# Kernel tuning notes

Measured on AMD Instinct MI355X. Metric: run time of the kernel, lower is better.

Reference implementation:

```python
import jax, jax.numpy as jnp
import numpy as np

# NF4 codebook used by bitsandbytes (16 levels, normalized to [-1, 1])
NF4_CODE = jnp.array([
    -1.0, -0.6961928009986877, -0.5250730514526367, -0.39491748809814453,
    -0.28444138169288635, -0.18477343022823334, -0.09105003625154495, 0.0,
    0.07958029955625534, 0.16093020141124725, 0.24611230194568634,
    0.33791524171829224, 0.44070982933044434, 0.5626170039176941,
    0.7229568362236023, 1.0], dtype=jnp.float32)
BLOCKSIZE = 64  # bitsandbytes default 4-bit blocksize


def nf4_quant_dequant(w):
    """Simulate bnb NF4 quantize -> dequantize (per-block absmax scaling)."""
    shape = w.shape
    flat = w.reshape(-1, BLOCKSIZE)                     # [n_blocks, 64]
    absmax = jnp.max(jnp.abs(flat), axis=1, keepdims=True)
    normalized = flat / jnp.where(absmax == 0, 1.0, absmax)
    # nearest-codebook-value quantization via midpoint boundaries
    bounds = (NF4_CODE[:-1] + NF4_CODE[1:]) * 0.5       # [15]
    idx = jnp.searchsorted(bounds, normalized)          # [n_blocks, 64] in [0,15]
    return (NF4_CODE[idx] * absmax).reshape(shape)


def setup_inputs() -> dict:
    key = jax.random.key(0)
    k1, k2, k3, kx = jax.random.split(key, 4)
    D, H = 4096, 11008
    scale = 0.02  # typical transformer init scale
    w1 = jax.random.normal(k1, (H, D), jnp.float32) * scale
    w2 = jax.random.normal(k2, (H, D), jnp.float32) * scale
    w3 = jax.random.normal(k3, (D, H), jnp.float32) * scale
    x = jax.random.normal(kx, (2, 2048, D), jnp.float32)
    return {"x": x, "w1": w1, "w2": w2, "w3": w3}


def reference(x, w1, w2, w3):
    dq1 = nf4_quant_dequant(w1)   # [H, D]
    dq2 = nf4_quant_dequant(w2)   # [H, D]
    dq3 = nf4_quant_dequant(w3)   # [D, H]
    gate = jnp.einsum('bsd,hd->bsh', x, dq1)
    up = jnp.einsum('bsd,hd->bsh', x, dq2)
    h = jax.nn.silu(gate) * up
    return jnp.einsum('bsh,dh->bsd', h, dq3)
```

## Files before the change

kernel.cpp:

```cpp
#include <hip/hip_runtime.h>
#include <math.h>

typedef __attribute__((ext_vector_type(4))) float f32x4;
typedef __attribute__((ext_vector_type(8))) short bf16x8;

#define DI __device__ __forceinline__

DI unsigned short f32_to_bf16(float f) {
  unsigned int u = __float_as_uint(f);
  u += 0x7FFFu + ((u >> 16) & 1u);
  return (unsigned short)(u >> 16);
}

static constexpr float kCode[16] = {
    -1.0f, -0.6961928009986877f, -0.5250730514526367f, -0.39491748809814453f,
    -0.28444138169288635f, -0.18477343022823334f, -0.09105003625154495f, 0.0f,
    0.07958029955625534f, 0.16093020141124725f, 0.24611230194568634f,
    0.33791524171829224f, 0.44070982933044434f, 0.5626170039176941f,
    0.7229568362236023f, 1.0f};

DI void dequant_body(const float* __restrict__ in, unsigned short* __restrict__ out, int i) {
  f32x4 v = reinterpret_cast<const f32x4*>(in)[i];
  float am = fmaxf(fmaxf(fabsf(v.x), fabsf(v.y)), fmaxf(fabsf(v.z), fabsf(v.w)));
  am = fmaxf(am, __shfl_xor(am, 1));
  am = fmaxf(am, __shfl_xor(am, 2));
  am = fmaxf(am, __shfl_xor(am, 4));
  am = fmaxf(am, __shfl_xor(am, 8));
  const float scale = (am == 0.0f) ? 1.0f : am;
  float sb[15];
#pragma unroll
  for (int b = 0; b < 15; ++b)
    sb[b] = (0.5f * (kCode[b] + kCode[b + 1])) * scale;
  unsigned short o[4];
#pragma unroll
  for (int j = 0; j < 4; ++j) {
    const float vj = ((const float*)&v)[j];
    int idx = 0;
#pragma unroll
    for (int b = 0; b < 15; ++b)
      idx += (vj > sb[b]) ? 1 : 0;
    o[j] = f32_to_bf16(kCode[idx] * am);
  }
  reinterpret_cast<ushort4*>(out)[i] = make_ushort4(o[0], o[1], o[2], o[3]);
}

__global__ void __launch_bounds__(256) k_dequant_nf4(
    const float* __restrict__ in, unsigned short* __restrict__ out, int n4) {
  int i = blockIdx.x * 256 + threadIdx.x;
  if (i >= n4) return;
  dequant_body(in, out, i);
}

__global__ void __launch_bounds__(256) k_aux_all(
    const float* __restrict__ x, unsigned short* __restrict__ xb, int n4x,
    const float* __restrict__ w1, unsigned short* __restrict__ w1b,
    const float* __restrict__ w2, unsigned short* __restrict__ w2b, int n4w) {
  int i = blockIdx.x * 256 + threadIdx.x;
  if (i < n4x) {
    f32x4 v = reinterpret_cast<const f32x4*>(x)[i];
    reinterpret_cast<ushort4*>(xb)[i] =
        make_ushort4(f32_to_bf16(v.x), f32_to_bf16(v.y), f32_to_bf16(v.z), f32_to_bf16(v.w));
  } else if (i < n4x + n4w) {
    dequant_body(w1, w1b, i - n4x);
  } else {
    dequant_body(w2, w2b, i - n4x - n4w);
  }
}

DI void gload16(const void* g, void* l) {
  __builtin_amdgcn_global_load_lds(
      (const __attribute__((address_space(1))) void*)g,
      (__attribute__((address_space(3))) void*)l, 16, 0, 0);
}

DI void barrier_nodrain() {
  asm volatile("" ::: "memory");
  __builtin_amdgcn_s_barrier();
  asm volatile("" ::: "memory");
}

#define WAITV(N) asm volatile("s_waitcnt vmcnt(" #N ")" ::: "memory")

DI float fast_silu(float g) {
  const float e = __builtin_amdgcn_exp2f(g * -1.442695041f);
  return g * __builtin_amdgcn_rcpf(1.0f + e);
}

__global__ void __launch_bounds__(1024, 4) k_gemm_dual_swiglu(
    const unsigned short* __restrict__ X,
    const unsigned short* __restrict__ W1,
    const unsigned short* __restrict__ W2,
    unsigned short* __restrict__ H) {
  constexpr int K = 4096, N = 11008, NK = K / 32;
  __shared__ char ldsb[131072];

  const int tid = threadIdx.x;
  const int w = tid >> 6, l = tid & 63;

  const int bid = blockIdx.x;
  const int xcd = bid & 7, ii = bid >> 3;
  const int nt = ii >> 1;
  const int mt = xcd * 2 + (ii & 1);
  const int m0 = mt * 256, n0 = nt * 128;

  const int p = w & 7;
  const bool isGate = (w < 8);
  const int wr = p >> 1, wc = p & 1;

  const int lrow = l >> 2;
  const int kc8 = (((l & 3) ^ ((l >> 3) & 3)) << 3);
  const unsigned short* gsrc0;
  const unsigned short* gsrc1;
  int ldst0;
  if (w < 8) {
    gsrc0 = X + (size_t)(m0 + 32 * w + lrow) * K + kc8;
    gsrc1 = X + (size_t)(m0 + 32 * w + 16 + lrow) * K + kc8;
    ldst0 = 2 * w * 1024;
  } else if (w < 12) {
    gsrc0 = W1 + (size_t)(n0 + 32 * (w - 8) + lrow) * K + kc8;
    gsrc1 = W1 + (size_t)(n0 + 32 * (w - 8) + 16 + lrow) * K + kc8;
    ldst0 = 16384 + (w - 8) * 2048;
  } else {
    gsrc0 = W2 + (size_t)(n0 + 32 * (w - 12) + lrow) * K + kc8;
    gsrc1 = W2 + (size_t)(n0 + 32 * (w - 12) + 16 + lrow) * K + kc8;
    ldst0 = 24576 + (w - 12) * 2048;
  }

  const int roff = (((l >> 4) ^ ((l >> 1) & 3)) << 4);
  const char* rdA = ldsb + (wr * 64 + (l & 15)) * 64 + roff;
  const char* rdB = ldsb + 16384 + (isGate ? 0 : 8192) +
                    (wc * 64 + (l & 15)) * 64 + roff;

  f32x4 acc[4][4] = {};

#define TILE_BODY(bo) {                                                        \
  bf16x8 a[4], b[4];                                                           \
  _Pragma("unroll") for (int m = 0; m < 4; ++m)                                \
    a[m] = *(const bf16x8*)(rdA + (bo) + m * 1024);                            \
  _Pragma("unroll") for (int n = 0; n < 4; ++n)                                \
    b[n] = *(const bf16x8*)(rdB + (bo) + n * 1024);                            \
  _Pragma("unroll") for (int m = 0; m < 4; ++m)                                \
    _Pragma("unroll") for (int n = 0; n < 4; ++n)                              \
      acc[m][n] = __builtin_amdgcn_mfma_f32_16x16x32_bf16(a[m], b[n], acc[m][n], 0, 0, 0); }

  gload16(gsrc0, ldsb + ldst0);               gload16(gsrc1, ldsb + ldst0 + 1024);
  gload16(gsrc0 + 32, ldsb + 32768 + ldst0);  gload16(gsrc1 + 32, ldsb + 32768 + ldst0 + 1024);
  gload16(gsrc0 + 64, ldsb + 65536 + ldst0);  gload16(gsrc1 + 64, ldsb + 65536 + ldst0 + 1024);
  const unsigned short* pg0 = gsrc0 + 96;
  const unsigned short* pg1 = gsrc1 + 96;
  WAITV(4);
  barrier_nodrain();

  int t = 0;
  for (; t + 3 < NK; ++t) {
    const int bo = (t & 3) << 15;
    const int bs = ((t + 3) & 3) << 15;
    gload16(pg0, ldsb + bs + ldst0);
    gload16(pg1, ldsb + bs + ldst0 + 1024);
    pg0 += 32; pg1 += 32;
    TILE_BODY(bo);
    WAITV(4); barrier_nodrain();
  }
  TILE_BODY((t & 3) << 15); WAITV(2); barrier_nodrain(); ++t;
  TILE_BODY((t & 3) << 15); WAITV(0); barrier_nodrain(); ++t;
  TILE_BODY((t & 3) << 15);
#undef TILE_BODY

  barrier_nodrain();
  char* xch = ldsb + p * 16384 + (isGate ? 0 : 8192);
#pragma unroll
  for (int m2 = 0; m2 < 2; ++m2)
#pragma unroll
    for (int n = 0; n < 4; ++n) {
      const int m = isGate ? (m2 + 2) : m2;
      *(f32x4*)(xch + ((m2 * 4 + n) * 64 + l) * 16) = acc[m][n];
    }
  barrier_nodrain();
  const char* oxch = ldsb + p * 16384 + (isGate ? 8192 : 0);
  const int er = (l >> 4) * 4, ec = l & 15;
#pragma unroll
  for (int m2 = 0; m2 < 2; ++m2)
#pragma unroll
    for (int n = 0; n < 4; ++n) {
      const int mk = isGate ? m2 : (m2 + 2);
      f32x4 other = *(const f32x4*)(oxch + ((m2 * 4 + n) * 64 + l) * 16);
#pragma unroll
      for (int j = 0; j < 4; ++j) {
        const float g_ = isGate ? acc[mk][n][j] : other[j];
        const float u_ = isGate ? other[j] : acc[mk][n][j];
        const float s = fast_silu(g_);
        const int row = m0 + wr * 64 + mk * 16 + er + j;
        const int col = n0 + wc * 64 + n * 16 + ec;
        H[(size_t)row * N + col] = f32_to_bf16(s * u_);
      }
    }
}

__global__ void __launch_bounds__(1024, 4) k_gemm_out(
    const unsigned short* __restrict__ Hm,
    const unsigned short* __restrict__ W3,
    float* __restrict__ Out) {
  constexpr int K = 11008, N = 4096, NK = K / 32;
  __shared__ char ldsb[131072];

  const int tid = threadIdx.x;
  const int w = tid >> 6, l = tid & 63;

  const int bid = blockIdx.x;
  const int xcd = bid & 7, ii = bid >> 3;
  const int nt = ii >> 1;
  const int mt = xcd * 2 + (ii & 1);
  const int m0 = mt * 256, n0 = nt * 256;

  const int wr = w >> 2, wc = w & 3;

  const int lrow = l >> 2;
  const int kc8 = (((l & 3) ^ ((l >> 3) & 3)) << 3);
  const unsigned short* gsrc0;
  const unsigned short* gsrc1;
  int ldst0;
  if (w < 8) {
    gsrc0 = Hm + (size_t)(m0 + 32 * w + lrow) * K + kc8;
    gsrc1 = Hm + (size_t)(m0 + 32 * w + 16 + lrow) * K + kc8;
    ldst0 = 2 * w * 1024;
  } else {
    gsrc0 = W3 + (size_t)(n0 + 32 * (w - 8) + lrow) * K + kc8;
    gsrc1 = W3 + (size_t)(n0 + 32 * (w - 8) + 16 + lrow) * K + kc8;
    ldst0 = 16384 + (w - 8) * 2048;
  }

  const int roff = (((l >> 4) ^ ((l >> 1) & 3)) << 4);
  const char* rdA = ldsb + (wr * 64 + (l & 15)) * 64 + roff;
  const char* rdB = ldsb + 16384 + (wc * 64 + (l & 15)) * 64 + roff;

  f32x4 acc[4][4] = {};

#define TILE_BODY(bo) {                                                        \
  bf16x8 a[4], b[4];                                                           \
  _Pragma("unroll") for (int m = 0; m < 4; ++m)                                \
    a[m] = *(const bf16x8*)(rdA + (bo) + m * 1024);                            \
  _Pragma("unroll") for (int n = 0; n < 4; ++n)                                \
    b[n] = *(const bf16x8*)(rdB + (bo) + n * 1024);                            \
  _Pragma("unroll") for (int m = 0; m < 4; ++m)                                \
    _Pragma("unroll") for (int n = 0; n < 4; ++n)                              \
      acc[m][n] = __builtin_amdgcn_mfma_f32_16x16x32_bf16(a[m], b[n], acc[m][n], 0, 0, 0); }

  gload16(gsrc0, ldsb + ldst0);               gload16(gsrc1, ldsb + ldst0 + 1024);
  gload16(gsrc0 + 32, ldsb + 32768 + ldst0);  gload16(gsrc1 + 32, ldsb + 32768 + ldst0 + 1024);
  gload16(gsrc0 + 64, ldsb + 65536 + ldst0);  gload16(gsrc1 + 64, ldsb + 65536 + ldst0 + 1024);
  const unsigned short* pg0 = gsrc0 + 96;
  const unsigned short* pg1 = gsrc1 + 96;
  WAITV(4);
  barrier_nodrain();

  int t = 0;
  for (; t + 3 < NK; ++t) {
    const int bo = (t & 3) << 15;
    const int bs = ((t + 3) & 3) << 15;
    gload16(pg0, ldsb + bs + ldst0);
    gload16(pg1, ldsb + bs + ldst0 + 1024);
    pg0 += 32; pg1 += 32;
    TILE_BODY(bo);
    WAITV(4); barrier_nodrain();
  }
  TILE_BODY((t & 3) << 15); WAITV(2); barrier_nodrain(); ++t;
  TILE_BODY((t & 3) << 15); WAITV(0); barrier_nodrain(); ++t;
  TILE_BODY((t & 3) << 15);
#undef TILE_BODY

  const int er = (l >> 4) * 4, ec = l & 15;
#pragma unroll
  for (int m = 0; m < 4; ++m)
#pragma unroll
    for (int n = 0; n < 4; ++n) {
      const int row = m0 + wr * 64 + m * 16 + er;
      const int col = n0 + wc * 64 + n * 16 + ec;
      float* ptr = Out + (size_t)row * N + col;
#pragma unroll
      for (int j = 0; j < 4; ++j) ptr[(size_t)j * N] = acc[m][n][j];
    }
}

extern "C" void kernel_launch(void* const* d_in, const int* in_sizes, int n_in,
                              void* d_out, int out_size, void* d_ws, size_t ws_size,
                              hipStream_t stream) {
  const float* x  = (const float*)d_in[0];
  const float* w1 = (const float*)d_in[1];
  const float* w2 = (const float*)d_in[2];
  const float* w3 = (const float*)d_in[3];
  float* out = (float*)d_out;

  char* ws = (char*)d_ws;
  unsigned short* xb  = (unsigned short*)(ws);
  unsigned short* w1b = (unsigned short*)(ws + 33554432);
  unsigned short* w2b = (unsigned short*)(ws + 123731968);
  unsigned short* hb  = (unsigned short*)(ws + 213909504);
  unsigned short* w3b = w1b;

  const int N4X = 4096 * 4096 / 4;
  const int NW  = 11008 * 4096 / 4;
  const int AUX_BLOCKS = (N4X + 2 * NW) / 256;
  k_aux_all<<<AUX_BLOCKS, 256, 0, stream>>>(x, xb, N4X, w1, w1b, w2, w2b, NW);

  k_gemm_dual_swiglu<<<1376, 1024, 0, stream>>>(xb, w1b, w2b, hb);

  k_dequant_nf4<<<NW / 256, 256, 0, stream>>>(w3, w3b, NW);

  k_gemm_out<<<256, 1024, 0, stream>>>(hb, w3b, out);
}
```

Baseline: 1.212 ms.

## Fold w3 dequant into aux kernel and remap GEMM tile order

When the workspace is large enough, w3 is dequantized into its own buffer inside the same prologue kernel as x, w1 and w2, which removes one kernel launch and the serialization between the first and second GEMMs. Both GEMM kernels also change their block-to-tile mapping: each XCD now sweeps all N tiles for one M tile before moving to the other, instead of alternating M tiles. That mapping change is meant to improve L2 reuse of the weight tiles. The cost is a larger workspace requirement, and a fallback path keeps the old schedule when that space is not available.

Measured after the change: 1.269 ms. 4.7% more time.

```diff
diff --git a/kernel.cpp b/kernel.cpp
--- a/kernel.cpp
+++ b/kernel.cpp
@@ -67,6 +67,25 @@
   }
 }
 
+__global__ void __launch_bounds__(256) k_aux_all4(
+    const float* __restrict__ x, unsigned short* __restrict__ xb, int n4x,
+    const float* __restrict__ w1, unsigned short* __restrict__ w1b,
+    const float* __restrict__ w2, unsigned short* __restrict__ w2b,
+    const float* __restrict__ w3, unsigned short* __restrict__ w3b, int n4w) {
+  int i = blockIdx.x * 256 + threadIdx.x;
+  if (i < n4x) {
+    f32x4 v = reinterpret_cast<const f32x4*>(x)[i];
+    reinterpret_cast<ushort4*>(xb)[i] =
+        make_ushort4(f32_to_bf16(v.x), f32_to_bf16(v.y), f32_to_bf16(v.z), f32_to_bf16(v.w));
+  } else if (i < n4x + n4w) {
+    dequant_body(w1, w1b, i - n4x);
+  } else if (i < n4x + 2 * n4w) {
+    dequant_body(w2, w2b, i - n4x - n4w);
+  } else {
+    dequant_body(w3, w3b, i - n4x - 2 * n4w);
+  }
+}
+
 DI void gload16(const void* g, void* l) {
   __builtin_amdgcn_global_load_lds(
       (const __attribute__((address_space(1))) void*)g,
@@ -99,8 +118,9 @@
 
   const int bid = blockIdx.x;
   const int xcd = bid & 7, ii = bid >> 3;
-  const int nt = ii >> 1;
-  const int mt = xcd * 2 + (ii & 1);
+  const int half = (ii >= 86) ? 1 : 0;
+  const int nt = ii - half * 86;
+  const int mt = xcd * 2 + half;
   const int m0 = mt * 256, n0 = nt * 128;
 
   const int p = w & 7;
@@ -208,8 +228,9 @@
 
   const int bid = blockIdx.x;
   const int xcd = bid & 7, ii = bid >> 3;
-  const int nt = ii >> 1;
-  const int mt = xcd * 2 + (ii & 1);
+  const int half = (ii >= 16) ? 1 : 0;
+  const int nt = ii - half * 16;
+  const int mt = xcd * 2 + half;
   const int m0 = mt * 256, n0 = nt * 256;
 
   const int wr = w >> 2, wc = w & 3;
@@ -295,16 +316,25 @@
   unsigned short* w1b = (unsigned short*)(ws + 33554432);
   unsigned short* w2b = (unsigned short*)(ws + 123731968);
   unsigned short* hb  = (unsigned short*)(ws + 213909504);
-  unsigned short* w3b = w1b;
 
   const int N4X = 4096 * 4096 / 4;
   const int NW  = 11008 * 4096 / 4;
-  const int AUX_BLOCKS = (N4X + 2 * NW) / 256;
-  k_aux_all<<<AUX_BLOCKS, 256, 0, stream>>>(x, xb, N4X, w1, w1b, w2, w2b, NW);
-
-  k_gemm_dual_swiglu<<<1376, 1024, 0, stream>>>(xb, w1b, w2b, hb);
-
-  k_dequant_nf4<<<NW / 256, 256, 0, stream>>>(w3, w3b, NW);
-
-  k_gemm_out<<<256, 1024, 0, stream>>>(hb, w3b, out);
-}
+
+  const size_t W3B_OFF = 304087040;
+  const bool sep_w3 = (ws_size >= W3B_OFF + 90177536);
+
+  if (sep_w3) {
+    unsigned short* w3b = (unsigned short*)(ws + W3B_OFF);
+    const int AUX_BLOCKS = (N4X + 3 * NW) / 256;
+    k_aux_all4<<<AUX_BLOCKS, 256, 0, stream>>>(x, xb, N4X, w1, w1b, w2, w2b, w3, w3b, NW);
+    k_gemm_dual_swiglu<<<1376, 1024, 0, stream>>>(xb, w1b, w2b, hb);
+    k_gemm_out<<<256, 1024, 0, stream>>>(hb, w3b, out);
+  } else {
+    unsigned short* w3b = w1b;
+    const int AUX_BLOCKS = (N4X + 2 * NW) / 256;
+    k_aux_all<<<AUX_BLOCKS, 256, 0, stream>>>(x, xb, N4X, w1, w1b, w2, w2b, NW);
+    k_gemm_dual_swiglu<<<1376, 1024, 0, stream>>>(xb, w1b, w2b, hb);
+    k_dequant_nf4<<<NW / 256, 256, 0, stream>>>(w3, w3b, NW);
+    k_gemm_out<<<256, 1024, 0, stream>>>(hb, w3b, out);
+  }
+}
```
